# Optimization experiments

Hardware: AMD Instinct MI355X
Metric: run time of the kernel (lower is better)

The kernel has to match this reference:

```python
import jax, jax.numpy as jnp
import numpy as np

N = 20000
E = 320000
IN_F = 128
HEADS = 8
OUT_F = 32
NEG_SLOPE = 0.2


def setup_inputs() -> dict:
    key = jax.random.key(0)
    k = jax.random.split(key, 8)
    x = jax.random.normal(k[0], (N, IN_F), dtype=jnp.float32)
    edge_index = jax.random.randint(k[1], (2, E), 0, N, dtype=jnp.int32)
    # Linear weights stored torch-style: [out, in]
    scale = 1.0 / np.sqrt(IN_F)
    W = jax.random.normal(k[2], (HEADS * OUT_F, IN_F), dtype=jnp.float32) * scale
    W1 = jax.random.normal(k[3], (HEADS * OUT_F, IN_F), dtype=jnp.float32) * scale
    W2 = jax.random.normal(k[4], (HEADS * OUT_F, IN_F), dtype=jnp.float32) * scale
    att = jax.random.normal(k[5], (1, HEADS, OUT_F), dtype=jnp.float32) * 0.1
    bias = jnp.zeros((HEADS * OUT_F,), dtype=jnp.float32)
    return {"x": x, "edge_index": edge_index, "W": W, "W1": W1, "W2": W2,
            "att": att, "bias": bias}


def reference(x, edge_index, W, W1, W2, att, bias):
    n, heads, out_f = x.shape[0], att.shape[1], att.shape[2]
    src, dst = edge_index[0], edge_index[1]

    # Node projections: [N, H, F]
    h_src = (x @ W1.T).reshape(n, heads, out_f)
    h_dst = (x @ W2.T).reshape(n, heads, out_f)
    values = (x @ W.T).reshape(n, heads, out_f)

    # Edge-wise GATv2 logits: a^T LeakyReLU(W1 h_i + W2 h_j)  -> [E, H]
    att_input = jax.nn.leaky_relu(h_src[src] + h_dst[dst], negative_slope=NEG_SLOPE)
    logits = jnp.einsum('ehf,hf->eh', att_input, att[0])

    # Segment softmax over incoming edges of each dst node (stable).
    seg_max = jax.ops.segment_max(logits, dst, num_segments=n)  # [N, H]
    exp_l = jnp.exp(logits - seg_max[dst])
    denom = jax.ops.segment_sum(exp_l, dst, num_segments=n)     # [N, H]
    weights = exp_l / denom[dst]                                # [E, H]

    # Weighted aggregation of source values into dst nodes.
    weighted = weights[:, :, None] * values[src]                # [E, H, F]
    out = jax.ops.segment_sum(weighted, dst, num_segments=n)    # [N, H, F]

    out = out.reshape(n, heads * out_f) + bias
    return out
```

## Files before the change

kernel.cpp:

```cpp
#include <hip/hip_runtime.h>
#include <math.h>

#define NN 20000
#define EE 320000
#define KF 128
#define HO 256
#define CAP 96

typedef __attribute__((ext_vector_type(8))) short short8;
typedef __attribute__((ext_vector_type(4))) float f32x4;

static __device__ __forceinline__ unsigned short f2bf(float f) {
    union { float f; unsigned u; } v; v.f = f;
    unsigned u = v.u;
    u += 0x7fffu + ((u >> 16) & 1u);
    return (unsigned short)(u >> 16);
}
static __device__ __forceinline__ float bf2f(unsigned short b) {
    union { unsigned u; float f; } v; v.u = ((unsigned)b) << 16;
    return v.f;
}

__global__ __launch_bounds__(256) void prep_kernel(
    const float* __restrict__ W0, const float* __restrict__ W1,
    const float* __restrict__ W2, unsigned short* __restrict__ whl,
    int* __restrict__ cursor)
{
    const int b = blockIdx.x;
    const int t = threadIdx.x;
    if (b < 96) {
        const int m = b >> 5;
        const float* __restrict__ Wm = (m == 0) ? W0 : (m == 1) ? W1 : W2;
        int idx = ((b & 31) * 256 + t) * 4;
        float4 v = *(const float4*)(Wm + idx);
        ushort4 h4, l4;
        h4.x = f2bf(v.x); l4.x = f2bf(v.x - bf2f(h4.x));
        h4.y = f2bf(v.y); l4.y = f2bf(v.y - bf2f(h4.y));
        h4.z = f2bf(v.z); l4.z = f2bf(v.z - bf2f(h4.z));
        h4.w = f2bf(v.w); l4.w = f2bf(v.w - bf2f(h4.w));
        *(ushort4*)(whl + (size_t)(m * 2 + 0) * 256 * 128 + idx) = h4;
        *(ushort4*)(whl + (size_t)(m * 2 + 1) * 256 * 128 + idx) = l4;
    } else {
        int i = (b - 96) * 256 + t;
        if (i < NN) cursor[i] = 0;
    }
}

__global__ void scatter_kernel(const int* __restrict__ ei, int* __restrict__ cursor,
                               int* __restrict__ csr_src) {
    int e = blockIdx.x * blockDim.x + threadIdx.x;
    if (e < EE) {
        int s = ei[e];
        int d = ei[EE + e];
        int pos = atomicAdd(&cursor[d], 1);
        if (pos < CAP) csr_src[d * CAP + pos] = s;
    }
}

__global__ __launch_bounds__(256, 2) void proj_kernel(
    const float* __restrict__ x, const unsigned short* __restrict__ whl,
    unsigned short* __restrict__ values, unsigned short* __restrict__ hsrc,
    unsigned short* __restrict__ hdst)
{
    const int m = blockIdx.y;
    unsigned short* __restrict__ dst = (m == 0) ? values : (m == 1) ? hsrc : hdst;
    const unsigned short* __restrict__ wh = whl + (size_t)(m * 2 + 0) * 256 * 128;
    const unsigned short* __restrict__ wl = whl + (size_t)(m * 2 + 1) * 256 * 128;

    const int nb   = blockIdx.x * 128;
    const int w    = threadIdx.x >> 6;
    const int lane = threadIdx.x & 63;
    const int lr   = lane & 15;
    const int q    = lane >> 4;

    f32x4 acc[2][16];
#pragma unroll
    for (int mi = 0; mi < 2; ++mi)
#pragma unroll
        for (int nt = 0; nt < 16; ++nt) acc[mi][nt] = (f32x4){0.f, 0.f, 0.f, 0.f};

    const int r0 = nb + w * 32;

    for (int ks = 0; ks < 4; ++ks) {
        const int kcol = ks * 32 + q * 8;
        short8 a_h[2], a_l[2];
#pragma unroll
        for (int mi = 0; mi < 2; ++mi) {
            const int row = r0 + mi * 16 + lr;
            float4 xa = make_float4(0.f, 0.f, 0.f, 0.f), xb = xa;
            if (row < NN) {
                const float* xp = x + (size_t)row * KF + kcol;
                xa = *(const float4*)xp;
                xb = *(const float4*)(xp + 4);
            }
            float xv[8] = {xa.x, xa.y, xa.z, xa.w, xb.x, xb.y, xb.z, xb.w};
#pragma unroll
            for (int j = 0; j < 8; ++j) {
                unsigned short h = f2bf(xv[j]);
                a_h[mi][j] = (short)h;
                a_l[mi][j] = (short)f2bf(xv[j] - bf2f(h));
            }
        }
#pragma unroll
        for (int nt = 0; nt < 16; ++nt) {
            size_t bo = (size_t)(nt * 16 + lr) * KF + kcol;
            short8 b_h = *(const short8*)(wh + bo);
            short8 b_l = *(const short8*)(wl + bo);
#pragma unroll
            for (int mi = 0; mi < 2; ++mi) {
                acc[mi][nt] = __builtin_amdgcn_mfma_f32_16x16x32_bf16(a_h[mi], b_h, acc[mi][nt], 0, 0, 0);
                acc[mi][nt] = __builtin_amdgcn_mfma_f32_16x16x32_bf16(a_h[mi], b_l, acc[mi][nt], 0, 0, 0);
                acc[mi][nt] = __builtin_amdgcn_mfma_f32_16x16x32_bf16(a_l[mi], b_h, acc[mi][nt], 0, 0, 0);
            }
        }
    }

#pragma unroll
    for (int mi = 0; mi < 2; ++mi) {
        const int rbase = r0 + mi * 16 + q * 4;
#pragma unroll
        for (int r = 0; r < 4; ++r) {
            const int row = rbase + r;
            if (row < NN) {
#pragma unroll
                for (int nt = 0; nt < 16; ++nt)
                    dst[(size_t)row * HO + nt * 16 + lr] = f2bf(acc[mi][nt][r]);
            }
        }
    }
}

__global__ __launch_bounds__(256) void gat_kernel(
    const unsigned short* __restrict__ hsrc, const unsigned short* __restrict__ hdst,
    const unsigned short* __restrict__ values, const float* __restrict__ att,
    const float* __restrict__ bias, const int* __restrict__ cursor,
    const int* __restrict__ csr_src, float* __restrict__ out)
{
    const int w    = threadIdx.x >> 6;
    const int d    = blockIdx.x * 4 + w;
    const int lane = threadIdx.x & 63;
    const int col  = lane * 4;

    const float4 a4 = *(const float4*)(att + col);
    const float4 b4 = *(const float4*)(bias + col);
    const ushort4 hd4 = *(const ushort4*)(hdst + (size_t)d * HO + col);
    const float hd0 = bf2f(hd4.x), hd1 = bf2f(hd4.y), hd2 = bf2f(hd4.z), hd3 = bf2f(hd4.w);

    int deg = cursor[d];
    if (deg > CAP) deg = CAP;

    int sreg = (lane < deg) ? csr_src[d * CAP + lane] : 0;

    float l = 0.f;
    float o0 = 0.f, o1 = 0.f, o2 = 0.f, o3 = 0.f;

#define EDGE_CALC(HV, VV)                                                     \
    {                                                                         \
        float z0 = bf2f(HV.x) + hd0, z1 = bf2f(HV.y) + hd1;                   \
        float z2 = bf2f(HV.z) + hd2, z3 = bf2f(HV.w) + hd3;                   \
        z0 = fmaxf(z0, 0.2f * z0); z1 = fmaxf(z1, 0.2f * z1);                 \
        z2 = fmaxf(z2, 0.2f * z2); z3 = fmaxf(z3, 0.2f * z3);                 \
        float p = fmaf(a4.x, z0, a4.y * z1) + fmaf(a4.z, z2, a4.w * z3);      \
        p += __shfl_xor(p, 1); p += __shfl_xor(p, 2); p += __shfl_xor(p, 4);  \
        const float e = __expf(p);                                            \
        l += e;                                                               \
        o0 = fmaf(e, bf2f(VV.x), o0);                                         \
        o1 = fmaf(e, bf2f(VV.y), o1);                                         \
        o2 = fmaf(e, bf2f(VV.z), o2);                                         \
        o3 = fmaf(e, bf2f(VV.w), o3);                                         \
    }

    const int nfast = (deg < 64) ? deg : 64;
    int i = 0;
    for (; i + 4 <= nfast; i += 4) {
        const int s0 = __shfl(sreg, i);
        const int s1 = __shfl(sreg, i + 1);
        const int s2 = __shfl(sreg, i + 2);
        const int s3 = __shfl(sreg, i + 3);
        const size_t r0_ = (size_t)s0 * HO + col;
        const size_t r1_ = (size_t)s1 * HO + col;
        const size_t r2_ = (size_t)s2 * HO + col;
        const size_t r3_ = (size_t)s3 * HO + col;
        const ushort4 hv0 = *(const ushort4*)(hsrc + r0_);
        const ushort4 vv0 = *(const ushort4*)(values + r0_);
        const ushort4 hv1 = *(const ushort4*)(hsrc + r1_);
        const ushort4 vv1 = *(const ushort4*)(values + r1_);
        const ushort4 hv2 = *(const ushort4*)(hsrc + r2_);
        const ushort4 vv2 = *(const ushort4*)(values + r2_);
        const ushort4 hv3 = *(const ushort4*)(hsrc + r3_);
        const ushort4 vv3 = *(const ushort4*)(values + r3_);
        EDGE_CALC(hv0, vv0);
        EDGE_CALC(hv1, vv1);
        EDGE_CALC(hv2, vv2);
        EDGE_CALC(hv3, vv3);
    }
    for (; i < nfast; ++i) {
        const int s0 = __shfl(sreg, i);
        const size_t r0_ = (size_t)s0 * HO + col;
        const ushort4 hv0 = *(const ushort4*)(hsrc + r0_);
        const ushort4 vv0 = *(const ushort4*)(values + r0_);
        EDGE_CALC(hv0, vv0);
    }
    for (int j = 64; j < deg; ++j) {
        const int s0 = csr_src[d * CAP + j];
        const size_t r0_ = (size_t)s0 * HO + col;
        const ushort4 hv0 = *(const ushort4*)(hsrc + r0_);
        const ushort4 vv0 = *(const ushort4*)(values + r0_);
        EDGE_CALC(hv0, vv0);
    }
#undef EDGE_CALC

    const float inv = (deg > 0) ? 1.f / l : 0.f;
    float4 res;
    res.x = o0 * inv + b4.x;
    res.y = o1 * inv + b4.y;
    res.z = o2 * inv + b4.z;
    res.w = o3 * inv + b4.w;
    *(float4*)(out + (size_t)d * HO + col) = res;
}

extern "C" void kernel_launch(void* const* d_in, const int* in_sizes, int n_in,
                              void* d_out, int out_size, void* d_ws, size_t ws_size,
                              hipStream_t stream) {
    const float* x    = (const float*)d_in[0];
    const int*   ei   = (const int*)d_in[1];
    const float* W0   = (const float*)d_in[2];
    const float* W1   = (const float*)d_in[3];
    const float* W2   = (const float*)d_in[4];
    const float* att  = (const float*)d_in[5];
    const float* bias = (const float*)d_in[6];
    float* out = (float*)d_out;

    char* p = (char*)d_ws;
    unsigned short* whl = (unsigned short*)p; p += (size_t)3 * 2 * 256 * 128 * 2;
    unsigned short* values = (unsigned short*)p; p += (size_t)NN * HO * 2;
    unsigned short* hsrc   = (unsigned short*)p; p += (size_t)NN * HO * 2;
    unsigned short* hdst   = (unsigned short*)p; p += (size_t)NN * HO * 2;
    int* cursor  = (int*)p; p += (size_t)NN * sizeof(int);
    int* csr_src = (int*)p; p += (size_t)NN * CAP * sizeof(int);

    prep_kernel<<<175, 256, 0, stream>>>(W0, W1, W2, whl, cursor);
    scatter_kernel<<<(EE + 255) / 256, 256, 0, stream>>>(ei, cursor, csr_src);
    proj_kernel<<<dim3((NN + 127) / 128, 3), 256, 0, stream>>>(x, whl, values, hsrc, hdst);
    gat_kernel<<<NN / 4, 256, 0, stream>>>(hsrc, hdst, values, att, bias, cursor, csr_src, out);
}
```

Measured before the change: 177.8 us.

## Use single-pass bf16 projection, fuse prep into proj, interleave hsrc/values rows

Drops the split-bf16 (hi/lo) three-MFMA emulation of fp32 matmul in favour of a single bf16 MFMA per tile, converting weights on the fly. This removes the separate prep kernel by folding cursor zeroing into the projection kernel. hsrc and values are stored interleaved in one 512-wide row so each gathered edge touches one contiguous 1KB span. The gat kernel is also relaunched with 128-thread blocks. Lower precision in the projections may raise error against the fp32 reference.

Result: no change. 175.6 us (-1.2%).

```diff
diff --git a/kernel.cpp b/kernel.cpp
--- a/kernel.cpp
+++ b/kernel.cpp
@@ -21,28 +21,81 @@
     return v.f;
 }
 
-__global__ __launch_bounds__(256) void prep_kernel(
-    const float* __restrict__ W0, const float* __restrict__ W1,
-    const float* __restrict__ W2, unsigned short* __restrict__ whl,
+__global__ __launch_bounds__(256, 2) void proj_kernel(
+    const float* __restrict__ x, const float* __restrict__ W0,
+    const float* __restrict__ W1, const float* __restrict__ W2,
+    unsigned short* __restrict__ hv, unsigned short* __restrict__ hdst,
     int* __restrict__ cursor)
 {
-    const int b = blockIdx.x;
-    const int t = threadIdx.x;
-    if (b < 96) {
-        const int m = b >> 5;
-        const float* __restrict__ Wm = (m == 0) ? W0 : (m == 1) ? W1 : W2;
-        int idx = ((b & 31) * 256 + t) * 4;
-        float4 v = *(const float4*)(Wm + idx);
-        ushort4 h4, l4;
-        h4.x = f2bf(v.x); l4.x = f2bf(v.x - bf2f(h4.x));
-        h4.y = f2bf(v.y); l4.y = f2bf(v.y - bf2f(h4.y));
-        h4.z = f2bf(v.z); l4.z = f2bf(v.z - bf2f(h4.z));
-        h4.w = f2bf(v.w); l4.w = f2bf(v.w - bf2f(h4.w));
-        *(ushort4*)(whl + (size_t)(m * 2 + 0) * 256 * 128 + idx) = h4;
-        *(ushort4*)(whl + (size_t)(m * 2 + 1) * 256 * 128 + idx) = l4;
-    } else {
-        int i = (b - 96) * 256 + t;
+    const int m = blockIdx.y;
+    const float* __restrict__ Wm = (m == 0) ? W0 : (m == 1) ? W1 : W2;
+    unsigned short* __restrict__ dst = (m == 0) ? (hv + 256) : (m == 1) ? hv : hdst;
+    const int stride = (m == 2) ? 256 : 512;
+
+    if (m == 0 && blockIdx.x < 79) {
+        int i = blockIdx.x * 256 + threadIdx.x;
         if (i < NN) cursor[i] = 0;
+    }
+
+    const int nb   = blockIdx.x * 128;
+    const int w    = threadIdx.x >> 6;
+    const int lane = threadIdx.x & 63;
+    const int lr   = lane & 15;
+    const int q    = lane >> 4;
+
+    f32x4 acc[2][16];
+#pragma unroll
+    for (int mi = 0; mi < 2; ++mi)
+#pragma unroll
+        for (int nt = 0; nt < 16; ++nt) acc[mi][nt] = (f32x4){0.f, 0.f, 0.f, 0.f};
+
+    const int r0 = nb + w * 32;
+
+    for (int ks = 0; ks < 4; ++ks) {
+        const int kcol = ks * 32 + q * 8;
+        short8 a_f[2];
+#pragma unroll
+        for (int mi = 0; mi < 2; ++mi) {
+            const int row = r0 + mi * 16 + lr;
+            float4 xa = make_float4(0.f, 0.f, 0.f, 0.f), xb = xa;
+            if (row < NN) {
+                const float* xp = x + (size_t)row * KF + kcol;
+                xa = *(const float4*)xp;
+                xb = *(const float4*)(xp + 4);
+            }
+            a_f[mi][0] = (short)f2bf(xa.x); a_f[mi][1] = (short)f2bf(xa.y);
+            a_f[mi][2] = (short)f2bf(xa.z); a_f[mi][3] = (short)f2bf(xa.w);
+            a_f[mi][4] = (short)f2bf(xb.x); a_f[mi][5] = (short)f2bf(xb.y);
+            a_f[mi][6] = (short)f2bf(xb.z); a_f[mi][7] = (short)f2bf(xb.w);
+        }
+#pragma unroll
+        for (int nt = 0; nt < 16; ++nt) {
+            const float* wp = Wm + (size_t)(nt * 16 + lr) * KF + kcol;
+            float4 wa = *(const float4*)wp;
+            float4 wb = *(const float4*)(wp + 4);
+            short8 b_f;
+            b_f[0] = (short)f2bf(wa.x); b_f[1] = (short)f2bf(wa.y);
+            b_f[2] = (short)f2bf(wa.z); b_f[3] = (short)f2bf(wa.w);
+            b_f[4] = (short)f2bf(wb.x); b_f[5] = (short)f2bf(wb.y);
+            b_f[6] = (short)f2bf(wb.z); b_f[7] = (short)f2bf(wb.w);
+#pragma unroll
+            for (int mi = 0; mi < 2; ++mi)
+                acc[mi][nt] = __builtin_amdgcn_mfma_f32_16x16x32_bf16(a_f[mi], b_f, acc[mi][nt], 0, 0, 0);
+        }
+    }
+
+#pragma unroll
+    for (int mi = 0; mi < 2; ++mi) {
+        const int rbase = r0 + mi * 16 + q * 4;
+#pragma unroll
+        for (int r = 0; r < 4; ++r) {
+            const int row = rbase + r;
+            if (row < NN) {
+#pragma unroll
+                for (int nt = 0; nt < 16; ++nt)
+                    dst[(size_t)row * stride + nt * 16 + lr] = f2bf(acc[mi][nt][r]);
+            }
+        }
     }
 }
 
@@ -57,87 +110,14 @@
     }
 }
 
-__global__ __launch_bounds__(256, 2) void proj_kernel(
-    const float* __restrict__ x, const unsigned short* __restrict__ whl,
-    unsigned short* __restrict__ values, unsigned short* __restrict__ hsrc,
-    unsigned short* __restrict__ hdst)
-{
-    const int m = blockIdx.y;
-    unsigned short* __restrict__ dst = (m == 0) ? values : (m == 1) ? hsrc : hdst;
-    const unsigned short* __restrict__ wh = whl + (size_t)(m * 2 + 0) * 256 * 128;
-    const unsigned short* __restrict__ wl = whl + (size_t)(m * 2 + 1) * 256 * 128;
-
-    const int nb   = blockIdx.x * 128;
-    const int w    = threadIdx.x >> 6;
-    const int lane = threadIdx.x & 63;
-    const int lr   = lane & 15;
-    const int q    = lane >> 4;
-
-    f32x4 acc[2][16];
-#pragma unroll
-    for (int mi = 0; mi < 2; ++mi)
-#pragma unroll
-        for (int nt = 0; nt < 16; ++nt) acc[mi][nt] = (f32x4){0.f, 0.f, 0.f, 0.f};
-
-    const int r0 = nb + w * 32;
-
-    for (int ks = 0; ks < 4; ++ks) {
-        const int kcol = ks * 32 + q * 8;
-        short8 a_h[2], a_l[2];
-#pragma unroll
-        for (int mi = 0; mi < 2; ++mi) {
-            const int row = r0 + mi * 16 + lr;
-            float4 xa = make_float4(0.f, 0.f, 0.f, 0.f), xb = xa;
-            if (row < NN) {
-                const float* xp = x + (size_t)row * KF + kcol;
-                xa = *(const float4*)xp;
-                xb = *(const float4*)(xp + 4);
-            }
-            float xv[8] = {xa.x, xa.y, xa.z, xa.w, xb.x, xb.y, xb.z, xb.w};
-#pragma unroll
-            for (int j = 0; j < 8; ++j) {
-                unsigned short h = f2bf(xv[j]);
-                a_h[mi][j] = (short)h;
-                a_l[mi][j] = (short)f2bf(xv[j] - bf2f(h));
-            }
-        }
-#pragma unroll
-        for (int nt = 0; nt < 16; ++nt) {
-            size_t bo = (size_t)(nt * 16 + lr) * KF + kcol;
-            short8 b_h = *(const short8*)(wh + bo);
-            short8 b_l = *(const short8*)(wl + bo);
-#pragma unroll
-            for (int mi = 0; mi < 2; ++mi) {
-                acc[mi][nt] = __builtin_amdgcn_mfma_f32_16x16x32_bf16(a_h[mi], b_h, acc[mi][nt], 0, 0, 0);
-                acc[mi][nt] = __builtin_amdgcn_mfma_f32_16x16x32_bf16(a_h[mi], b_l, acc[mi][nt], 0, 0, 0);
-                acc[mi][nt] = __builtin_amdgcn_mfma_f32_16x16x32_bf16(a_l[mi], b_h, acc[mi][nt], 0, 0, 0);
-            }
-        }
-    }
-
-#pragma unroll
-    for (int mi = 0; mi < 2; ++mi) {
-        const int rbase = r0 + mi * 16 + q * 4;
-#pragma unroll
-        for (int r = 0; r < 4; ++r) {
-            const int row = rbase + r;
-            if (row < NN) {
-#pragma unroll
-                for (int nt = 0; nt < 16; ++nt)
-                    dst[(size_t)row * HO + nt * 16 + lr] = f2bf(acc[mi][nt][r]);
-            }
-        }
-    }
-}
-
-__global__ __launch_bounds__(256) void gat_kernel(
-    const unsigned short* __restrict__ hsrc, const unsigned short* __restrict__ hdst,
-    const unsigned short* __restrict__ values, const float* __restrict__ att,
-    const float* __restrict__ bias, const int* __restrict__ cursor,
-    const int* __restrict__ csr_src, float* __restrict__ out)
+__global__ __launch_bounds__(128) void gat_kernel(
+    const unsigned short* __restrict__ hv, const unsigned short* __restrict__ hdst,
+    const float* __restrict__ att, const float* __restrict__ bias,
+    const int* __restrict__ cursor, const int* __restrict__ csr_src,
+    float* __restrict__ out)
 {
     const int w    = threadIdx.x >> 6;
-    const int d    = blockIdx.x * 4 + w;
+    const int d    = blockIdx.x * 2 + w;
     const int lane = threadIdx.x & 63;
     const int col  = lane * 4;
 
@@ -177,18 +157,18 @@
         const int s1 = __shfl(sreg, i + 1);
         const int s2 = __shfl(sreg, i + 2);
         const int s3 = __shfl(sreg, i + 3);
-        const size_t r0_ = (size_t)s0 * HO + col;
-        const size_t r1_ = (size_t)s1 * HO + col;
-        const size_t r2_ = (size_t)s2 * HO + col;
-        const size_t r3_ = (size_t)s3 * HO + col;
-        const ushort4 hv0 = *(const ushort4*)(hsrc + r0_);
-        const ushort4 vv0 = *(const ushort4*)(values + r0_);
-        const ushort4 hv1 = *(const ushort4*)(hsrc + r1_);
-        const ushort4 vv1 = *(const ushort4*)(values + r1_);
-        const ushort4 hv2 = *(const ushort4*)(hsrc + r2_);
-        const ushort4 vv2 = *(const ushort4*)(values + r2_);
-        const ushort4 hv3 = *(const ushort4*)(hsrc + r3_);
-        const ushort4 vv3 = *(const ushort4*)(values + r3_);
+        const unsigned short* p0 = hv + (size_t)s0 * 512 + col;
+        const unsigned short* p1 = hv + (size_t)s1 * 512 + col;
+        const unsigned short* p2 = hv + (size_t)s2 * 512 + col;
+        const unsigned short* p3 = hv + (size_t)s3 * 512 + col;
+        const ushort4 hv0 = *(const ushort4*)p0;
+        const ushort4 vv0 = *(const ushort4*)(p0 + 256);
+        const ushort4 hv1 = *(const ushort4*)p1;
+        const ushort4 vv1 = *(const ushort4*)(p1 + 256);
+        const ushort4 hv2 = *(const ushort4*)p2;
+        const ushort4 vv2 = *(const ushort4*)(p2 + 256);
+        const ushort4 hv3 = *(const ushort4*)p3;
+        const ushort4 vv3 = *(const ushort4*)(p3 + 256);
         EDGE_CALC(hv0, vv0);
         EDGE_CALC(hv1, vv1);
         EDGE_CALC(hv2, vv2);
@@ -196,16 +176,16 @@
     }
     for (; i < nfast; ++i) {
         const int s0 = __shfl(sreg, i);
-        const size_t r0_ = (size_t)s0 * HO + col;
-        const ushort4 hv0 = *(const ushort4*)(hsrc + r0_);
-        const ushort4 vv0 = *(const ushort4*)(values + r0_);
+        const unsigned short* p0 = hv + (size_t)s0 * 512 + col;
+        const ushort4 hv0 = *(const ushort4*)p0;
+        const ushort4 vv0 = *(const ushort4*)(p0 + 256);
         EDGE_CALC(hv0, vv0);
     }
     for (int j = 64; j < deg; ++j) {
         const int s0 = csr_src[d * CAP + j];
-        const size_t r0_ = (size_t)s0 * HO + col;
-        const ushort4 hv0 = *(const ushort4*)(hsrc + r0_);
-        const ushort4 vv0 = *(const ushort4*)(values + r0_);
+        const unsigned short* p0 = hv + (size_t)s0 * 512 + col;
+        const ushort4 hv0 = *(const ushort4*)p0;
+        const ushort4 vv0 = *(const ushort4*)(p0 + 256);
         EDGE_CALC(hv0, vv0);
     }
 #undef EDGE_CALC
@@ -232,15 +212,12 @@
     float* out = (float*)d_out;
 
     char* p = (char*)d_ws;
-    unsigned short* whl = (unsigned short*)p; p += (size_t)3 * 2 * 256 * 128 * 2;
-    unsigned short* values = (unsigned short*)p; p += (size_t)NN * HO * 2;
-    unsigned short* hsrc   = (unsigned short*)p; p += (size_t)NN * HO * 2;
-    unsigned short* hdst   = (unsigned short*)p; p += (size_t)NN * HO * 2;
+    unsigned short* hv   = (unsigned short*)p; p += (size_t)NN * 512 * 2;
+    unsigned short* hdst = (unsigned short*)p; p += (size_t)NN * HO * 2;
     int* cursor  = (int*)p; p += (size_t)NN * sizeof(int);
     int* csr_src = (int*)p; p += (size_t)NN * CAP * sizeof(int);
 
-    prep_kernel<<<175, 256, 0, stream>>>(W0, W1, W2, whl, cursor);
+    proj_kernel<<<dim3((NN + 127) / 128, 3), 256, 0, stream>>>(x, W0, W1, W2, hv, hdst, cursor);
     scatter_kernel<<<(EE + 255) / 256, 256, 0, stream>>>(ei, cursor, csr_src);
-    proj_kernel<<<dim3((NN + 127) / 128, 3), 256, 0, stream>>>(x, whl, values, hsrc, hdst);
-    gat_kernel<<<NN / 4, 256, 0, stream>>>(hsrc, hdst, values, att, bias, cursor, csr_src, out);
-}
+    gat_kernel<<<NN / 2, 128, 0, stream>>>(hv, hdst, att, bias, cursor, csr_src, out);
+}
```
